# Optimization experiments

Measured on AMD Instinct MI355X. Metric: run time of the kernel, lower is better.

Reference implementation:

```python
import jax, jax.numpy as jnp
import numpy as np

B, S, D, H = 8192, 4, 2048, 16
HD = D // H
LN_EPS = 1e-5
NUM_PATH = 4


def setup_inputs() -> dict:
    key = jax.random.key(0)
    ks = jax.random.split(key, 12)
    scale = 1.0 / np.sqrt(D)
    inp = {
        "seq_feats": jax.random.normal(ks[0], (B, S, D), dtype=jnp.float32),
        "seq_available": jnp.ones((B, S), dtype=bool),
        "pathology_idx": 1,
        # pathology-specific query projections, stacked [num_pathologies, D, D]
        "Wq": jax.random.normal(ks[1], (NUM_PATH, D, D), dtype=jnp.float32) * scale,
        "bq": jnp.zeros((NUM_PATH, D), dtype=jnp.float32),
        "Wk": jax.random.normal(ks[2], (D, D), dtype=jnp.float32) * scale,
        "bk": jnp.zeros((D,), dtype=jnp.float32),
        "Wv": jax.random.normal(ks[3], (D, D), dtype=jnp.float32) * scale,
        "bv": jnp.zeros((D,), dtype=jnp.float32),
        "Wo": jax.random.normal(ks[4], (D, D), dtype=jnp.float32) * scale,
        "bo": jnp.zeros((D,), dtype=jnp.float32),
        "gamma": jnp.ones((D,), dtype=jnp.float32),
        "beta": jnp.zeros((D,), dtype=jnp.float32),
    }
    return inp


def reference(seq_feats, seq_available, pathology_idx, Wq, bq, Wk, bk, Wv, bv, Wo, bo, gamma, beta):
    # seq_feats: [B, S, D]; seq_available: [B, S] bool
    query_input = seq_feats.mean(axis=1)                      # [B, D]
    Q = query_input @ Wq[pathology_idx] + bq[pathology_idx]   # [B, D]
    K = seq_feats @ Wk + bk                                   # [B, S, D]
    V = seq_feats @ Wv + bv                                   # [B, S, D]

    Qh = Q.reshape(B, H, HD)          # [B, H, hd] (single query token)
    Kh = K.reshape(B, S, H, HD)
    Vh = V.reshape(B, S, H, HD)

    scores = jnp.einsum("bhd,bshd->bhs", Qh, Kh) / np.sqrt(HD)  # [B, H, S]
    # masked_fill(~available, -inf)
    scores = jnp.where(seq_available[:, None, :], scores, -jnp.inf)
    attn = jax.nn.softmax(scores, axis=-1)                        # [B, H, S]
    # dropout is identity in eval / p=0
    ctx = jnp.einsum("bhs,bshd->bhd", attn, Vh).reshape(B, D)     # [B, D]
    out = ctx @ Wo + bo                                           # [B, D]

    # LayerNorm
    mu = out.mean(axis=-1, keepdims=True)
    var = out.var(axis=-1, keepdims=True)
    out = (out - mu) * jax.lax.rsqrt(var + LN_EPS) * gamma + beta
    return out
```

## Files before the change

### kernel.cpp

```cpp
#include <hip/hip_runtime.h>


typedef __attribute__((ext_vector_type(8))) short    bf16x8;
typedef __attribute__((ext_vector_type(4))) float    f32x4;
typedef __attribute__((ext_vector_type(4))) unsigned short u16x4;

#define DIM 2048
constexpr int Bsz = 8192;
constexpr int Ssz = 4;
constexpr int Hn  = 16;

__device__ __forceinline__ unsigned short f2bf(float x) {
    unsigned u = __float_as_uint(x);
    u += 0x7FFFu + ((u >> 16) & 1u);
    return (unsigned short)(u >> 16);
}

__device__ __forceinline__ void gll16(const void* g, void* l) {
    __builtin_amdgcn_global_load_lds(
        (const __attribute__((address_space(1))) unsigned int*)g,
        (__attribute__((address_space(3))) unsigned int*)l,
        16, 0, 0);
}

__global__ __launch_bounds__(256) void convert_seq(
    const float* __restrict__ seq,
    unsigned short* __restrict__ shi, unsigned short* __restrict__ qhi)
{
    const int b  = blockIdx.x;
    const int d0 = blockIdx.y * 1024 + threadIdx.x * 4;
    const size_t base = (size_t)b * Ssz * DIM + d0;
    float m0 = 0.f, m1 = 0.f, m2 = 0.f, m3 = 0.f;
#pragma unroll
    for (int s = 0; s < Ssz; ++s) {
        const float4 v = *(const float4*)(seq + base + (size_t)s * DIM);
        m0 += v.x; m1 += v.y; m2 += v.z; m3 += v.w;
        u16x4 h;
        h.x = f2bf(v.x); h.y = f2bf(v.y); h.z = f2bf(v.z); h.w = f2bf(v.w);
        *(u16x4*)(shi + base + (size_t)s * DIM) = h;
    }
    u16x4 h;
    h.x = f2bf(m0 * 0.25f); h.y = f2bf(m1 * 0.25f);
    h.z = f2bf(m2 * 0.25f); h.w = f2bf(m3 * 0.25f);
    *(u16x4*)(qhi + (size_t)b * DIM + d0) = h;
}

__global__ __launch_bounds__(256) void convert_w(
    const float* __restrict__ Wq, const float* __restrict__ Wk,
    const float* __restrict__ Wv, const float* __restrict__ Wo,
    const int* __restrict__ pidx,
    unsigned short* __restrict__ thi)
{
    __shared__ float tile[32][33];
    const int z = blockIdx.z;
    const float* W = Wq + (size_t)(*pidx) * DIM * DIM;
    if (z == 1) W = Wk; else if (z == 2) W = Wv; else if (z == 3) W = Wo;
    unsigned short* Th = thi + (size_t)z * DIM * DIM;
    const int n0 = blockIdx.x * 32, k0 = blockIdx.y * 32;
    const int tx = threadIdx.x, ty = threadIdx.y;
#pragma unroll
    for (int i = 0; i < 4; ++i)
        tile[ty + i * 8][tx] = W[(size_t)(k0 + ty + i * 8) * DIM + n0 + tx];
    __syncthreads();
#pragma unroll
    for (int i = 0; i < 4; ++i)
        Th[(size_t)(n0 + ty + i * 8) * DIM + k0 + tx] = f2bf(tile[tx][ty + i * 8]);
}

template <int EPI>
__global__ __launch_bounds__(256, 2) void gemm_bt(
    const unsigned short* __restrict__ A, const unsigned short* __restrict__ Bm,
    const float* __restrict__ bias, const int* __restrict__ pidx, const int bias_stride,
    float* __restrict__ Cout,
    const float* __restrict__ Qmat, float* __restrict__ scores,
    const float* __restrict__ attn, unsigned short* __restrict__ ctx)
{
    constexpr int K = DIM, N = DIM;
    alignas(16) __shared__ unsigned short lds[8192];
    unsigned short* lA = lds;
    unsigned short* lB = lds + 4096;

    const int tid  = threadIdx.x;
    const int lane = tid & 63;
    const int lr   = lane & 15;
    const int lkb  = lane >> 4;
    const int w    = tid >> 6;
    const int wm   = w >> 1, wn = w & 1;
    const int row_base = blockIdx.y * 128;
    const int col_base = blockIdx.x * 128;

    f32x4 acc[4][4] = {};

    for (int kt = 0; kt < K / 32; ++kt) {
        const int k0 = kt * 32;
#pragma unroll
        for (int i = 0; i < 2; ++i) {
            const int idx = i * 256 + tid;
            const int r   = idx >> 2;
            const int kc  = (idx & 3) * 8;
            gll16(A  + (size_t)(row_base + r) * K + k0 + kc, lA + idx * 8);
            gll16(Bm + (size_t)(col_base + r) * K + k0 + kc, lB + idx * 8);
        }
        __syncthreads();

        bf16x8 ah[4], bh[4];
#pragma unroll
        for (int mi = 0; mi < 4; ++mi)
            ah[mi] = *(const bf16x8*)(lA + (wm * 64 + mi * 16 + lr) * 32 + lkb * 8);
#pragma unroll
        for (int ni = 0; ni < 4; ++ni)
            bh[ni] = *(const bf16x8*)(lB + (wn * 64 + ni * 16 + lr) * 32 + lkb * 8);
#pragma unroll
        for (int mi = 0; mi < 4; ++mi)
#pragma unroll
            for (int ni = 0; ni < 4; ++ni)
                acc[mi][ni] = __builtin_amdgcn_mfma_f32_16x16x32_bf16(ah[mi], bh[ni], acc[mi][ni], 0, 0, 0);
        __syncthreads();
    }

    if constexpr (EPI == 0) {
        const int p = *pidx;
        const float* bp = bias + (size_t)p * bias_stride;
#pragma unroll
        for (int ni = 0; ni < 4; ++ni) {
            const int col = col_base + wn * 64 + ni * 16 + lr;
            const float bb = bp[col];
#pragma unroll
            for (int mi = 0; mi < 4; ++mi)
#pragma unroll
                for (int j = 0; j < 4; ++j) {
                    const int row = row_base + wm * 64 + mi * 16 + lkb * 4 + j;
                    Cout[(size_t)row * N + col] = acc[mi][ni][j] + bb;
                }
        }
    } else if constexpr (EPI == 1) {
        const int h = blockIdx.x;
        float part[4][4];
#pragma unroll
        for (int mi = 0; mi < 4; ++mi) {
#pragma unroll
            for (int j = 0; j < 4; ++j) {
                const int grow = row_base + wm * 64 + mi * 16 + lkb * 4 + j;
                const int b = grow >> 2;
                float sum = 0.f;
#pragma unroll
                for (int ni = 0; ni < 4; ++ni) {
                    const int col = col_base + wn * 64 + ni * 16 + lr;
                    sum += (acc[mi][ni][j] + bias[col]) * Qmat[(size_t)b * DIM + col];
                }
#pragma unroll
                for (int off = 1; off < 16; off <<= 1)
                    sum += __shfl_xor(sum, off, 64);
                part[mi][j] = sum;
            }
        }
        float* red = (float*)lds;
        if (lr == 0) {
#pragma unroll
            for (int mi = 0; mi < 4; ++mi)
#pragma unroll
                for (int j = 0; j < 4; ++j) {
                    const int rl = wm * 64 + mi * 16 + lkb * 4 + j;
                    red[rl * 2 + wn] = part[mi][j];
                }
        }
        __syncthreads();
        if (tid < 128) {
            const int grow = row_base + tid;
            const float s = (red[tid * 2] + red[tid * 2 + 1]) * 0.08838834764831845f;
            scores[(size_t)((grow >> 2) * Hn + h) * Ssz + (grow & 3)] = s;
        }
    } else {
        const int h = blockIdx.x;
#pragma unroll
        for (int mi = 0; mi < 4; ++mi) {
            const int rbase = row_base + wm * 64 + mi * 16 + lkb * 4;
            const int b = rbase >> 2;
            const float4 at = *(const float4*)(attn + (size_t)(b * Hn + h) * Ssz);
#pragma unroll
            for (int ni = 0; ni < 4; ++ni) {
                const int col = col_base + wn * 64 + ni * 16 + lr;
                const float bb = bias[col];
                const float c = at.x * (acc[mi][ni][0] + bb) + at.y * (acc[mi][ni][1] + bb)
                              + at.z * (acc[mi][ni][2] + bb) + at.w * (acc[mi][ni][3] + bb);
                ctx[(size_t)b * DIM + col] = f2bf(c);
            }
        }
    }
}

__global__ __launch_bounds__(256) void softmax_k(
    const float* __restrict__ scores, const int* __restrict__ avail,
    float* __restrict__ attn)
{
    const int i = blockIdx.x * 256 + threadIdx.x;
    const int b = i >> 4;
    const float4 sc = ((const float4*)scores)[i];
    const int4 am = ((const int4*)avail)[b];
    const float NI = -__builtin_inff();
    const float s0 = am.x ? sc.x : NI;
    const float s1 = am.y ? sc.y : NI;
    const float s2 = am.z ? sc.z : NI;
    const float s3 = am.w ? sc.w : NI;
    const float m  = fmaxf(fmaxf(s0, s1), fmaxf(s2, s3));
    const float e0 = expf(s0 - m), e1 = expf(s1 - m), e2 = expf(s2 - m), e3 = expf(s3 - m);
    const float inv = 1.0f / (e0 + e1 + e2 + e3);
    float4 r; r.x = e0 * inv; r.y = e1 * inv; r.z = e2 * inv; r.w = e3 * inv;
    ((float4*)attn)[i] = r;
}

__global__ __launch_bounds__(256) void ln_kernel(
    const float* __restrict__ in, const float* __restrict__ gamma,
    const float* __restrict__ beta, float* __restrict__ out)
{
    __shared__ float red[8];
    const int row = blockIdx.x, t = threadIdx.x;
    const float4* r4 = (const float4*)(in + (size_t)row * DIM);
    const float4 a = r4[t], b = r4[t + 256];
    float s = a.x + a.y + a.z + a.w + b.x + b.y + b.z + b.w;
#pragma unroll
    for (int o = 32; o > 0; o >>= 1) s += __shfl_down(s, o, 64);
    if ((t & 63) == 0) red[t >> 6] = s;
    __syncthreads();
    const float mean = (red[0] + red[1] + red[2] + red[3]) * (1.0f / DIM);
    float q = 0.f, dx;
    dx = a.x - mean; q += dx * dx;  dx = a.y - mean; q += dx * dx;
    dx = a.z - mean; q += dx * dx;  dx = a.w - mean; q += dx * dx;
    dx = b.x - mean; q += dx * dx;  dx = b.y - mean; q += dx * dx;
    dx = b.z - mean; q += dx * dx;  dx = b.w - mean; q += dx * dx;
#pragma unroll
    for (int o = 32; o > 0; o >>= 1) q += __shfl_down(q, o, 64);
    if ((t & 63) == 0) red[4 + (t >> 6)] = q;
    __syncthreads();
    const float var = (red[4] + red[5] + red[6] + red[7]) * (1.0f / DIM);
    const float rs = 1.0f / sqrtf(var + 1e-5f);
    const float4* g4  = (const float4*)gamma;
    const float4* be4 = (const float4*)beta;
    const float4 g = g4[t], be = be4[t], g2 = g4[t + 256], be2 = be4[t + 256];
    float4 o1, o2;
    o1.x = (a.x - mean) * rs * g.x + be.x;   o1.y = (a.y - mean) * rs * g.y + be.y;
    o1.z = (a.z - mean) * rs * g.z + be.z;   o1.w = (a.w - mean) * rs * g.w + be.w;
    o2.x = (b.x - mean) * rs * g2.x + be2.x; o2.y = (b.y - mean) * rs * g2.y + be2.y;
    o2.z = (b.z - mean) * rs * g2.z + be2.z; o2.w = (b.w - mean) * rs * g2.w + be2.w;
    float4* o4 = (float4*)(out + (size_t)row * DIM);
    o4[t] = o1; o4[t + 256] = o2;
}

extern "C" void kernel_launch(void* const* d_in, const int* in_sizes, int n_in,
                              void* d_out, int out_size, void* d_ws, size_t ws_size,
                              hipStream_t stream)
{
    const float* seq   = (const float*)d_in[0];
    const int*   avail = (const int*)d_in[1];
    const int*   pidx  = (const int*)d_in[2];
    const float* Wq    = (const float*)d_in[3];
    const float* bq    = (const float*)d_in[4];
    const float* Wk    = (const float*)d_in[5];
    const float* bk    = (const float*)d_in[6];
    const float* Wv    = (const float*)d_in[7];
    const float* bv    = (const float*)d_in[8];
    const float* Wo    = (const float*)d_in[9];
    const float* bo    = (const float*)d_in[10];
    const float* gamma = (const float*)d_in[11];
    const float* beta  = (const float*)d_in[12];
    float* out = (float*)d_out;

    char* ws = (char*)d_ws;
    size_t off = 0;
    auto alloc = [&](size_t bytes) -> void* {
        void* p = ws + off;
        off += (bytes + 255) & ~(size_t)255;
        return p;
    };
    unsigned short* seq_hi = (unsigned short*)alloc((size_t)Bsz * Ssz * DIM * 2);
    unsigned short* q_hi   = (unsigned short*)alloc((size_t)Bsz * DIM * 2);
    unsigned short* wt_hi  = (unsigned short*)alloc((size_t)4 * DIM * DIM * 2);
    float*          Qmat   = (float*)alloc((size_t)Bsz * DIM * 4);
    float*          scores = (float*)alloc((size_t)Bsz * Hn * Ssz * 4);
    float*          attn   = (float*)alloc((size_t)Bsz * Hn * Ssz * 4);
    unsigned short* ctx    = q_hi;
    float*          outpre = Qmat;

    const size_t DD = (size_t)DIM * DIM;

    convert_seq<<<dim3(Bsz, 2), 256, 0, stream>>>(seq, seq_hi, q_hi);
    convert_w<<<dim3(64, 64, 4), dim3(32, 8), 0, stream>>>(Wq, Wk, Wv, Wo, pidx, wt_hi);

    gemm_bt<0><<<dim3(16, 64), 256, 0, stream>>>(
        q_hi, wt_hi, bq, pidx, DIM,
        Qmat, nullptr, nullptr, nullptr, nullptr);
    gemm_bt<1><<<dim3(16, 256), 256, 0, stream>>>(
        seq_hi, wt_hi + DD, bk, pidx, 0,
        nullptr, Qmat, scores, nullptr, nullptr);
    softmax_k<<<dim3(512), 256, 0, stream>>>(scores, avail, attn);
    gemm_bt<2><<<dim3(16, 256), 256, 0, stream>>>(
        seq_hi, wt_hi + 2 * DD, bv, pidx, 0,
        nullptr, nullptr, nullptr, attn, ctx);
    gemm_bt<0><<<dim3(16, 64), 256, 0, stream>>>(
        ctx, wt_hi + 3 * DD, bo, pidx, 0,
        outpre, nullptr, nullptr, nullptr, nullptr);
    ln_kernel<<<dim3(Bsz), 256, 0, stream>>>(outpre, gamma, beta, out);
}
```

Before: 1.285 ms.

## Reorder attention-weighted V projection to combine sequence before the GEMM

```diff
diff --git a/kernel.cpp b/kernel.cpp
--- a/kernel.cpp
+++ b/kernel.cpp
@@ -21,6 +21,10 @@
         (const __attribute__((address_space(1))) unsigned int*)g,
         (__attribute__((address_space(3))) unsigned int*)l,
         16, 0, 0);
+}
+
+__device__ __forceinline__ int xcd_swz(int wg, int nwg) {
+    return (wg & 7) * (nwg >> 3) + (wg >> 3);
 }
 
 __global__ __launch_bounds__(256) void convert_seq(
@@ -72,13 +76,17 @@
     const unsigned short* __restrict__ A, const unsigned short* __restrict__ Bm,
     const float* __restrict__ bias, const int* __restrict__ pidx, const int bias_stride,
     float* __restrict__ Cout,
-    const float* __restrict__ Qmat, float* __restrict__ scores,
-    const float* __restrict__ attn, unsigned short* __restrict__ ctx)
+    const float* __restrict__ Qmat, float* __restrict__ scores)
 {
     constexpr int K = DIM, N = DIM;
     alignas(16) __shared__ unsigned short lds[8192];
     unsigned short* lA = lds;
     unsigned short* lB = lds + 4096;
+
+    const int nwg = gridDim.x * gridDim.y;
+    const int wg  = xcd_swz(blockIdx.y * gridDim.x + blockIdx.x, nwg);
+    const int bx  = wg % gridDim.x;
+    const int by  = wg / gridDim.x;
 
     const int tid  = threadIdx.x;
     const int lane = tid & 63;
@@ -86,8 +94,8 @@
     const int lkb  = lane >> 4;
     const int w    = tid >> 6;
     const int wm   = w >> 1, wn = w & 1;
-    const int row_base = blockIdx.y * 128;
-    const int col_base = blockIdx.x * 128;
+    const int row_base = by * 128;
+    const int col_base = bx * 128;
 
     f32x4 acc[4][4] = {};
 
@@ -133,8 +141,8 @@
                     Cout[(size_t)row * N + col] = acc[mi][ni][j] + bb;
                 }
         }
-    } else if constexpr (EPI == 1) {
-        const int h = blockIdx.x;
+    } else {
+        const int h = bx;
         float part[4][4];
 #pragma unroll
         for (int mi = 0; mi < 4; ++mi) {
@@ -170,22 +178,96 @@
             const float s = (red[tid * 2] + red[tid * 2 + 1]) * 0.08838834764831845f;
             scores[(size_t)((grow >> 2) * Hn + h) * Ssz + (grow & 3)] = s;
         }
-    } else {
-        const int h = blockIdx.x;
-#pragma unroll
-        for (int mi = 0; mi < 4; ++mi) {
-            const int rbase = row_base + wm * 64 + mi * 16 + lkb * 4;
-            const int b = rbase >> 2;
-            const float4 at = *(const float4*)(attn + (size_t)(b * Hn + h) * Ssz);
-#pragma unroll
-            for (int ni = 0; ni < 4; ++ni) {
-                const int col = col_base + wn * 64 + ni * 16 + lr;
-                const float bb = bias[col];
-                const float c = at.x * (acc[mi][ni][0] + bb) + at.y * (acc[mi][ni][1] + bb)
-                              + at.z * (acc[mi][ni][2] + bb) + at.w * (acc[mi][ni][3] + bb);
-                ctx[(size_t)b * DIM + col] = f2bf(c);
+    }
+}
+
+__global__ __launch_bounds__(256, 2) void gemm_av(
+    const unsigned short* __restrict__ seq,
+    const unsigned short* __restrict__ WvT,
+    const float* __restrict__ bv,
+    const float* __restrict__ attn,
+    unsigned short* __restrict__ ctx)
+{
+    alignas(16) __shared__ unsigned short lds[8192];
+    unsigned short* lA = lds;
+    unsigned short* lB = lds + 4096;
+
+    const int nwg = gridDim.x * gridDim.y;
+    const int wg  = xcd_swz(blockIdx.y * gridDim.x + blockIdx.x, nwg);
+    const int bx  = wg % gridDim.x;
+    const int by  = wg / gridDim.x;
+
+    const int tid  = threadIdx.x;
+    const int lane = tid & 63;
+    const int lr   = lane & 15;
+    const int lkb  = lane >> 4;
+    const int w    = tid >> 6;
+    const int wm   = w >> 1, wn = w & 1;
+    const int row_base = by * 128;
+    const int col_base = bx * 128;
+
+    const int rt = tid >> 1;
+    const int ch = (tid & 1) * 16;
+    const int bb = row_base + rt;
+    const float4 at4 = *(const float4*)(attn + ((size_t)bb * Hn + bx) * Ssz);
+    const float aw[4] = { at4.x, at4.y, at4.z, at4.w };
+    const unsigned short* srow = seq + (size_t)bb * Ssz * DIM;
+
+    f32x4 acc[4][4] = {};
+
+    for (int kt = 0; kt < DIM / 32; ++kt) {
+        const int k0 = kt * 32;
+#pragma unroll
+        for (int i = 0; i < 2; ++i) {
+            const int idx = i * 256 + tid;
+            gll16(WvT + (size_t)(col_base + (idx >> 2)) * DIM + k0 + (idx & 3) * 8,
+                  lB + idx * 8);
+        }
+        float f0[8] = {}, f1[8] = {};
+#pragma unroll
+        for (int s = 0; s < 4; ++s) {
+            const bf16x8 v0 = *(const bf16x8*)(srow + (size_t)s * DIM + k0 + ch);
+            const bf16x8 v1 = *(const bf16x8*)(srow + (size_t)s * DIM + k0 + ch + 8);
+            const float a = aw[s];
+#pragma unroll
+            for (int i = 0; i < 8; ++i) {
+                f0[i] += a * __uint_as_float(((unsigned)(unsigned short)v0[i]) << 16);
+                f1[i] += a * __uint_as_float(((unsigned)(unsigned short)v1[i]) << 16);
             }
         }
+        bf16x8 p0, p1;
+#pragma unroll
+        for (int i = 0; i < 8; ++i) { p0[i] = (short)f2bf(f0[i]); p1[i] = (short)f2bf(f1[i]); }
+        *(bf16x8*)(lA + rt * 32 + ch)     = p0;
+        *(bf16x8*)(lA + rt * 32 + ch + 8) = p1;
+        __syncthreads();
+
+        bf16x8 ah[4], bh[4];
+#pragma unroll
+        for (int mi = 0; mi < 4; ++mi)
+            ah[mi] = *(const bf16x8*)(lA + (wm * 64 + mi * 16 + lr) * 32 + lkb * 8);
+#pragma unroll
+        for (int ni = 0; ni < 4; ++ni)
+            bh[ni] = *(const bf16x8*)(lB + (wn * 64 + ni * 16 + lr) * 32 + lkb * 8);
+#pragma unroll
+        for (int mi = 0; mi < 4; ++mi)
+#pragma unroll
+            for (int ni = 0; ni < 4; ++ni)
+                acc[mi][ni] = __builtin_amdgcn_mfma_f32_16x16x32_bf16(ah[mi], bh[ni], acc[mi][ni], 0, 0, 0);
+        __syncthreads();
+    }
+
+#pragma unroll
+    for (int ni = 0; ni < 4; ++ni) {
+        const int col = col_base + wn * 64 + ni * 16 + lr;
+        const float bvc = bv[col];
+#pragma unroll
+        for (int mi = 0; mi < 4; ++mi)
+#pragma unroll
+            for (int j = 0; j < 4; ++j) {
+                const int row = row_base + wm * 64 + mi * 16 + lkb * 4 + j;
+                ctx[(size_t)row * DIM + col] = f2bf(acc[mi][ni][j] + bvc);
+            }
     }
 }
 
@@ -287,17 +369,13 @@
     convert_w<<<dim3(64, 64, 4), dim3(32, 8), 0, stream>>>(Wq, Wk, Wv, Wo, pidx, wt_hi);
 
     gemm_bt<0><<<dim3(16, 64), 256, 0, stream>>>(
-        q_hi, wt_hi, bq, pidx, DIM,
-        Qmat, nullptr, nullptr, nullptr, nullptr);
+        q_hi, wt_hi, bq, pidx, DIM, Qmat, nullptr, nullptr);
     gemm_bt<1><<<dim3(16, 256), 256, 0, stream>>>(
-        seq_hi, wt_hi + DD, bk, pidx, 0,
-        nullptr, Qmat, scores, nullptr, nullptr);
+        seq_hi, wt_hi + DD, bk, pidx, 0, nullptr, Qmat, scores);
     softmax_k<<<dim3(512), 256, 0, stream>>>(scores, avail, attn);
-    gemm_bt<2><<<dim3(16, 256), 256, 0, stream>>>(
-        seq_hi, wt_hi + 2 * DD, bv, pidx, 0,
-        nullptr, nullptr, nullptr, attn, ctx);
+    gemm_av<<<dim3(16, 64), 256, 0, stream>>>(
+        seq_hi, wt_hi + 2 * DD, bv, attn, ctx);
     gemm_bt<0><<<dim3(16, 64), 256, 0, stream>>>(
-        ctx, wt_hi + 3 * DD, bo, pidx, 0,
-        outpre, nullptr, nullptr, nullptr, nullptr);
+        ctx, wt_hi + 3 * DD, bo, pidx, 0, outpre, nullptr, nullptr);
     ln_kernel<<<dim3(Bsz), 256, 0, stream>>>(outpre, gamma, beta, out);
 }
```

Measured after the change: 1.196 ms. 1.07x faster.
